# Optimization experiments

Measured on AMD Instinct MI355X. Metric: run time of the kernel, lower is better.

## Reference

```python
import jax, jax.numpy as jnp
import numpy as np

# 8-neighborhood offsets (dy, dx) in the same order as the torch module,
# so bit i of the LBP code corresponds to offsets[i].
OFFSETS = ((-1, -1), (-1, 0), (-1, 1), (0, 1), (1, 1), (1, 0), (1, -1), (0, -1))
NUM_BINS = 256


def setup_inputs() -> dict:
    key = jax.random.key(0)
    x = jax.random.uniform(key, (64, 3, 512, 512), dtype=jnp.float32)
    return {"x": x}


def reference(x) -> jnp.ndarray:
    bs, _, H, W = x.shape
    # RGB -> grayscale, [bs, H, W]
    gray = 0.2989 * x[:, 0] + 0.587 * x[:, 1] + 0.114 * x[:, 2]
    # replicate-pad by 1 on each spatial side ('edge' == torch 'replicate')
    pad = jnp.pad(gray, ((0, 0), (1, 1), (1, 1)), mode="edge")

    # Accumulate the 8-bit LBP code directly (fuses the codes/weights pass).
    lbp = jnp.zeros((bs, H, W), dtype=jnp.int32)
    for i, (dy, dx) in enumerate(OFFSETS):
        neigh = pad[:, 1 + dy:1 + dy + H, 1 + dx:1 + dx + W]
        lbp = lbp + (neigh >= gray).astype(jnp.int32) * (1 << i)

    # 256-bin histogram per image via a single scatter-add (bincount-style),
    # replacing the O(256*H*W) looped equality sums of the original.
    batch_idx = jnp.arange(bs, dtype=jnp.int32)[:, None]          # [bs, 1]
    flat = lbp.reshape(bs, H * W)                                  # [bs, H*W]
    hist = jnp.zeros((bs, NUM_BINS), dtype=jnp.float32).at[batch_idx, flat].add(1.0)

    # L2-normalize each histogram.
    norm = jnp.sqrt(jnp.sum(hist * hist, axis=1, keepdims=True))
    return hist / (norm + 1e-6)
```

## Files before the change

kernel.cpp:

```cpp
#include <hip/hip_runtime.h>

#define IMG_H 512
#define IMG_W 512
#define PLANE (IMG_H * IMG_W)
#define NBATCH 64
#define NBINS 256
#define TSTRIP 16
#define WAVES_PER_BLOCK 4
#define STRIPS_PER_IMG (IMG_H / TSTRIP)
#define BLOCKS_PER_IMG (STRIPS_PER_IMG / WAVES_PER_BLOCK)

#define GRAY(rr, gg, bb) (0.2989f * (rr) + 0.587f * (gg) + 0.114f * (bb))

__global__ __launch_bounds__(256) void lbp_strip_kernel(const float* __restrict__ x,
                                                        float* __restrict__ ws) {
    __shared__ unsigned int lh[NBINS];
    const int tid = threadIdx.x;
    lh[tid] = 0u;
    __syncthreads();

    const int b     = blockIdx.y;
    const int wav   = tid >> 6;
    const int lane  = tid & 63;
    const int strip = blockIdx.x * WAVES_PER_BLOCK + wav;
    const int y0    = strip * TSTRIP;

    const float* rP = x + (size_t)b * 3 * PLANE;
    const float* gP = rP + PLANE;
    const float* bP = rP + 2 * PLANE;
    const int    cx = 8 * lane;

    float t_[10], m_[10], b_[10];

    #define LOADGRAY(arr, gy_)                                                     \
    do {                                                                           \
        int gy = (gy_);                                                            \
        gy = gy < 0 ? 0 : (gy > IMG_H - 1 ? IMG_H - 1 : gy);                       \
        size_t off = (size_t)gy * IMG_W + cx;                                      \
        float4 ra = *(const float4*)(rP + off), rb = *(const float4*)(rP + off + 4);\
        float4 ga = *(const float4*)(gP + off), gb = *(const float4*)(gP + off + 4);\
        float4 ba = *(const float4*)(bP + off), bb = *(const float4*)(bP + off + 4);\
        arr[1] = GRAY(ra.x, ga.x, ba.x); arr[2] = GRAY(ra.y, ga.y, ba.y);          \
        arr[3] = GRAY(ra.z, ga.z, ba.z); arr[4] = GRAY(ra.w, ga.w, ba.w);          \
        arr[5] = GRAY(rb.x, gb.x, bb.x); arr[6] = GRAY(rb.y, gb.y, bb.y);          \
        arr[7] = GRAY(rb.z, gb.z, bb.z); arr[8] = GRAY(rb.w, gb.w, bb.w);          \
        float lft = __shfl_up(arr[8], 1, 64);                                      \
        float rgt = __shfl_down(arr[1], 1, 64);                                    \
        arr[0] = (lane == 0)  ? arr[1] : lft;                                      \
        arr[9] = (lane == 63) ? arr[8] : rgt;                                      \
    } while (0)

    LOADGRAY(t_, y0 - 1);
    LOADGRAY(m_, y0);

    #pragma unroll 4
    for (int i = 0; i < TSTRIP; ++i) {
        LOADGRAY(b_, y0 + 1 + i);
        #pragma unroll
        for (int p = 0; p < 8; ++p) {
            const float ctr = m_[p + 1];
            unsigned code = 0u;
            code |= (t_[p    ] >= ctr) ? 1u   : 0u;
            code |= (t_[p + 1] >= ctr) ? 2u   : 0u;
            code |= (t_[p + 2] >= ctr) ? 4u   : 0u;
            code |= (m_[p + 2] >= ctr) ? 8u   : 0u;
            code |= (b_[p + 2] >= ctr) ? 16u  : 0u;
            code |= (b_[p + 1] >= ctr) ? 32u  : 0u;
            code |= (b_[p    ] >= ctr) ? 64u  : 0u;
            code |= (m_[p    ] >= ctr) ? 128u : 0u;
            atomicAdd(&lh[code], 1u);
        }
        #pragma unroll
        for (int k = 0; k < 10; ++k) { t_[k] = m_[k]; m_[k] = b_[k]; }
    }
    #undef LOADGRAY

    __syncthreads();
    ws[((size_t)b * BLOCKS_PER_IMG + blockIdx.x) * NBINS + tid] = (float)lh[tid];
}

__global__ __launch_bounds__(256) void finalize_kernel(const float* __restrict__ ws,
                                                       float* __restrict__ out) {
    const int b = blockIdx.x;
    const int t = threadIdx.x;
    float s = 0.0f;
    #pragma unroll
    for (int k = 0; k < BLOCKS_PER_IMG; ++k)
        s += ws[((size_t)b * BLOCKS_PER_IMG + k) * NBINS + t];
    float ss = s * s;
    #pragma unroll
    for (int o = 32; o > 0; o >>= 1) ss += __shfl_down(ss, o, 64);
    __shared__ float wsum[4];
    if ((t & 63) == 0) wsum[t >> 6] = ss;
    __syncthreads();
    float tot = wsum[0] + wsum[1] + wsum[2] + wsum[3];
    out[b * NBINS + t] = s / (sqrtf(tot) + 1e-6f);
}

extern "C" void kernel_launch(void* const* d_in, const int* in_sizes, int n_in,
                              void* d_out, int out_size, void* d_ws, size_t ws_size,
                              hipStream_t stream) {
    const float* x = (const float*)d_in[0];
    float* out = (float*)d_out;
    float* ws  = (float*)d_ws;

    dim3 grid(BLOCKS_PER_IMG, NBATCH);
    lbp_strip_kernel<<<grid, 256, 0, stream>>>(x, ws);

    finalize_kernel<<<NBATCH, 256, 0, stream>>>(ws, out);
}
```

Measured before the change: 38.73 us.

## Swizzle block order across XCDs and walk odd strips bottom-up for halo reuse

```diff
diff --git a/kernel.cpp b/kernel.cpp
--- a/kernel.cpp
+++ b/kernel.cpp
@@ -9,6 +9,7 @@
 #define WAVES_PER_BLOCK 4
 #define STRIPS_PER_IMG (IMG_H / TSTRIP)
 #define BLOCKS_PER_IMG (STRIPS_PER_IMG / WAVES_PER_BLOCK)
+#define NBLOCKS (BLOCKS_PER_IMG * NBATCH)
 
 #define GRAY(rr, gg, bb) (0.2989f * (rr) + 0.587f * (gg) + 0.114f * (bb))
 
@@ -19,10 +20,14 @@
     lh[tid] = 0u;
     __syncthreads();
 
-    const int b     = blockIdx.y;
+    const int lin = blockIdx.x;
+    const int sid = (lin & 7) * (NBLOCKS / 8) + (lin >> 3);
+    const int b   = sid >> 3;
+    const int bg  = sid & 7;
+
     const int wav   = tid >> 6;
     const int lane  = tid & 63;
-    const int strip = blockIdx.x * WAVES_PER_BLOCK + wav;
+    const int strip = bg * WAVES_PER_BLOCK + wav;
     const int y0    = strip * TSTRIP;
 
     const float* rP = x + (size_t)b * 3 * PLANE;
@@ -50,33 +55,50 @@
         arr[9] = (lane == 63) ? arr[8] : rgt;                                      \
     } while (0)
 
-    LOADGRAY(t_, y0 - 1);
-    LOADGRAY(m_, y0);
+    #define COMPUTE8()                                                             \
+    do {                                                                           \
+        _Pragma("unroll")                                                          \
+        for (int p = 0; p < 8; ++p) {                                              \
+            const float ctr = m_[p + 1];                                           \
+            unsigned code = 0u;                                                    \
+            code |= (t_[p    ] >= ctr) ? 1u   : 0u;                                \
+            code |= (t_[p + 1] >= ctr) ? 2u   : 0u;                                \
+            code |= (t_[p + 2] >= ctr) ? 4u   : 0u;                                \
+            code |= (m_[p + 2] >= ctr) ? 8u   : 0u;                                \
+            code |= (b_[p + 2] >= ctr) ? 16u  : 0u;                                \
+            code |= (b_[p + 1] >= ctr) ? 32u  : 0u;                                \
+            code |= (b_[p    ] >= ctr) ? 64u  : 0u;                                \
+            code |= (m_[p    ] >= ctr) ? 128u : 0u;                                \
+            atomicAdd(&lh[code], 1u);                                              \
+        }                                                                          \
+    } while (0)
 
-    #pragma unroll 4
-    for (int i = 0; i < TSTRIP; ++i) {
-        LOADGRAY(b_, y0 + 1 + i);
-        #pragma unroll
-        for (int p = 0; p < 8; ++p) {
-            const float ctr = m_[p + 1];
-            unsigned code = 0u;
-            code |= (t_[p    ] >= ctr) ? 1u   : 0u;
-            code |= (t_[p + 1] >= ctr) ? 2u   : 0u;
-            code |= (t_[p + 2] >= ctr) ? 4u   : 0u;
-            code |= (m_[p + 2] >= ctr) ? 8u   : 0u;
-            code |= (b_[p + 2] >= ctr) ? 16u  : 0u;
-            code |= (b_[p + 1] >= ctr) ? 32u  : 0u;
-            code |= (b_[p    ] >= ctr) ? 64u  : 0u;
-            code |= (m_[p    ] >= ctr) ? 128u : 0u;
-            atomicAdd(&lh[code], 1u);
+    if ((strip & 1) == 0) {
+        LOADGRAY(t_, y0 - 1);
+        LOADGRAY(m_, y0);
+        #pragma unroll 4
+        for (int i = 0; i < TSTRIP; ++i) {
+            LOADGRAY(b_, y0 + 1 + i);
+            COMPUTE8();
+            #pragma unroll
+            for (int k = 0; k < 10; ++k) { t_[k] = m_[k]; m_[k] = b_[k]; }
         }
-        #pragma unroll
-        for (int k = 0; k < 10; ++k) { t_[k] = m_[k]; m_[k] = b_[k]; }
+    } else {
+        LOADGRAY(b_, y0 + TSTRIP);
+        LOADGRAY(m_, y0 + TSTRIP - 1);
+        #pragma unroll 4
+        for (int i = 0; i < TSTRIP; ++i) {
+            LOADGRAY(t_, y0 + TSTRIP - 2 - i);
+            COMPUTE8();
+            #pragma unroll
+            for (int k = 0; k < 10; ++k) { b_[k] = m_[k]; m_[k] = t_[k]; }
+        }
     }
     #undef LOADGRAY
+    #undef COMPUTE8
 
     __syncthreads();
-    ws[((size_t)b * BLOCKS_PER_IMG + blockIdx.x) * NBINS + tid] = (float)lh[tid];
+    ws[((size_t)b * BLOCKS_PER_IMG + bg) * NBINS + tid] = (float)lh[tid];
 }
 
 __global__ __launch_bounds__(256) void finalize_kernel(const float* __restrict__ ws,
@@ -104,8 +126,6 @@
     float* out = (float*)d_out;
     float* ws  = (float*)d_ws;
 
-    dim3 grid(BLOCKS_PER_IMG, NBATCH);
-    lbp_strip_kernel<<<grid, 256, 0, stream>>>(x, ws);
-
+    lbp_strip_kernel<<<NBLOCKS, 256, 0, stream>>>(x, ws);
     finalize_kernel<<<NBATCH, 256, 0, stream>>>(ws, out);
 }
```

Result: faster. 37.88 us (-2.2%).
